# Kernel tuning notes

Measured on AMD Instinct MI355X. Metric: run time of the kernel, lower is better.

## Reference

```python
import jax, jax.numpy as jnp
import numpy as np

HIDDEN = 1024
NUM_HEADS = 16
HEAD_DIM = HIDDEN // NUM_HEADS
BATCH = 2
SEQ = 2048


def setup_inputs() -> dict:
    key = jax.random.key(0)
    k1, k2, k3 = jax.random.split(key, 3)
    hidden_states = jax.random.normal(k1, (BATCH, SEQ, HIDDEN), dtype=jnp.float32)
    attention_mask = jnp.zeros((BATCH, 1, SEQ, SEQ), dtype=jnp.float32)
    # nn.Linear weights: stored as [out_features, in_features]
    w_qkv = jax.random.normal(k2, (3 * HIDDEN, HIDDEN), dtype=jnp.float32) * (HIDDEN ** -0.5)
    w_o = jax.random.normal(k3, (HIDDEN, HIDDEN), dtype=jnp.float32) * (HIDDEN ** -0.5)
    return {"hidden_states": hidden_states, "attention_mask": attention_mask,
            "w_qkv": w_qkv, "w_o": w_o}


def reference(hidden_states, attention_mask, w_qkv, w_o):
    B, S, H = hidden_states.shape
    scale = HEAD_DIM ** -0.5
    qkv = jnp.einsum('bsh,oh->bso', hidden_states, w_qkv)  # [B,S,3H]
    qkv = qkv.reshape(B, S, 3, NUM_HEADS, HEAD_DIM)
    q = qkv[:, :, 0].transpose(0, 2, 1, 3)  # [B,nH,S,hd]
    k = qkv[:, :, 1].transpose(0, 2, 1, 3)
    v = qkv[:, :, 2].transpose(0, 2, 1, 3)
    attn = jnp.einsum('bhqd,bhkd->bhqk', q, k) * scale
    attn = attn + attention_mask
    attn = jax.nn.softmax(attn, axis=-1)
    out = jnp.einsum('bhqk,bhkd->bhqd', attn, v)
    out = out.transpose(0, 2, 1, 3).reshape(B, S, H)
    return jnp.einsum('bsh,oh->bso', out, w_o)
```

## Files before the change

kernel.cpp:

```cpp
#include <hip/hip_runtime.h>

typedef unsigned short u16;
using bf16x8 = __attribute__((ext_vector_type(8))) __bf16;
using f32x4  = __attribute__((ext_vector_type(4))) float;
using u16x8  = __attribute__((ext_vector_type(8))) unsigned short;
using u16x4  = __attribute__((ext_vector_type(4))) unsigned short;

#define SEQ   2048
#define HID   1024
#define NHEAD 16
#define HD    64
#define BATCH 2
#define NTOK  4096

__device__ __forceinline__ u16 f2bf(float f) {
  unsigned u = __builtin_bit_cast(unsigned, f);
  u += 0x7fffu + ((u >> 16) & 1u);
  return (u16)(u >> 16);
}

__device__ __forceinline__ void gld_lds16(const void* g, void* l) {
  __builtin_amdgcn_global_load_lds(
      (__attribute__((address_space(1))) void*)(__UINTPTR_TYPE__)g,
      (__attribute__((address_space(3))) void*)l, 16, 0, 0);
}

__global__ __launch_bounds__(256) void cvt_kernel(const float* __restrict__ in,
                                                  u16* __restrict__ out) {
  int i = (blockIdx.x * 256 + threadIdx.x) * 4;
  float4 v = *reinterpret_cast<const float4*>(in + i);
  u16x4 o = { f2bf(v.x), f2bf(v.y), f2bf(v.z), f2bf(v.w) };
  *reinterpret_cast<u16x4*>(out + i) = o;
}

template<bool BF16OUT>
__global__ __launch_bounds__(256) void gemm_bt(const u16* __restrict__ A,
                                               const u16* __restrict__ B,
                                               void* __restrict__ Cv,
                                               int M, int N, int K) {
  __shared__ u16 At[128 * 64];
  __shared__ u16 Bt[128 * 64];
  const int tid  = threadIdx.x;
  const int wave = tid >> 6;
  const int lane = tid & 63;
  const int g    = lane >> 4;
  const int r16  = lane & 15;
  const int wr   = wave >> 1;
  const int wc   = wave & 1;
  const int bm   = blockIdx.y;
  const int bn   = blockIdx.x;

  const u16* Ab = A + (size_t)bm * 128 * K;
  const u16* Bb = B + (size_t)bn * 128 * K;
  const int srow = lane >> 3;
  const int scol = (lane & 7) * 8;

  f32x4 acc[4][4] = {};

  for (int kt = 0; kt < K; kt += 64) {
#pragma unroll
    for (int c = 0; c < 4; ++c) {
      int seg = wave * 4 + c;
      gld_lds16(Ab + (size_t)(seg * 8 + srow) * K + kt + scol, &At[seg * 512]);
      gld_lds16(Bb + (size_t)(seg * 8 + srow) * K + kt + scol, &Bt[seg * 512]);
    }
    __syncthreads();
#pragma unroll
    for (int ko = 0; ko < 64; ko += 32) {
      bf16x8 af[4], bfr[4];
#pragma unroll
      for (int mi = 0; mi < 4; ++mi)
        af[mi] = *reinterpret_cast<const bf16x8*>(&At[(wr * 64 + mi * 16 + r16) * 64 + ko + g * 8]);
#pragma unroll
      for (int ni = 0; ni < 4; ++ni)
        bfr[ni] = *reinterpret_cast<const bf16x8*>(&Bt[(wc * 64 + ni * 16 + r16) * 64 + ko + g * 8]);
#pragma unroll
      for (int mi = 0; mi < 4; ++mi)
#pragma unroll
        for (int ni = 0; ni < 4; ++ni)
          acc[mi][ni] = __builtin_amdgcn_mfma_f32_16x16x32_bf16(af[mi], bfr[ni], acc[mi][ni], 0, 0, 0);
    }
    __syncthreads();
  }

#pragma unroll
  for (int mi = 0; mi < 4; ++mi)
#pragma unroll
    for (int ni = 0; ni < 4; ++ni) {
      int row0 = bm * 128 + wr * 64 + mi * 16 + g * 4;
      int col  = bn * 128 + wc * 64 + ni * 16 + r16;
#pragma unroll
      for (int r = 0; r < 4; ++r) {
        float v = acc[mi][ni][r];
        if (BF16OUT) ((u16*)Cv)[(size_t)(row0 + r) * N + col] = f2bf(v);
        else         ((float*)Cv)[(size_t)(row0 + r) * N + col] = v;
      }
    }
}

__global__ __launch_bounds__(256, 4) void attn_kernel(const u16* __restrict__ qkv,
                                                      const float* __restrict__ mask,
                                                      u16* __restrict__ AO) {
  __shared__ u16 Kt[2][64 * 64];
  __shared__ u16 Vt[64 * 64];
  __shared__ u16 Pl[4][16 * 64];

  const int tid  = threadIdx.x;
  const int w    = tid >> 6;
  const int lane = tid & 63;
  const int g    = lane >> 4;
  const int r16  = lane & 15;

  const int n  = blockIdx.x;
  const int x  = n & 7;
  const int s_ = n >> 3;
  const int h  = s_ & 15;
  const int t_ = ((s_ >> 4) << 3) + x;
  const int b  = t_ >> 5;
  const int qt = t_ & 31;

  const size_t tokbase = (size_t)b * SEQ;

  bf16x8 aq[2];
  {
    int qrow = qt * 64 + w * 16 + r16;
#pragma unroll
    for (int ko = 0; ko < 2; ++ko)
      aq[ko] = *reinterpret_cast<const bf16x8*>(
          qkv + ((tokbase + qrow) * 3 + 0) * HID + h * HD + ko * 32 + g * 8);
  }

  f32x4 o[4] = {};
  float mrow[4], lrow[4];
#pragma unroll
  for (int r = 0; r < 4; ++r) { mrow[r] = -3.0e38f; lrow[r] = 0.f; }

  const int srowK = lane >> 3;
  const int vkey  = tid >> 2;
  const int vd3   = tid & 3;

#define STAGE_K(buf, kb)                                                        \
  {                                                                             \
    _Pragma("unroll")                                                           \
    for (int c = 0; c < 2; ++c) {                                               \
      int seg = w * 2 + c;                                                      \
      int sK  = ((seg >> 1) + srowK) & 7;                                       \
      int srcc = (lane & 7) ^ sK;                                               \
      gld_lds16(qkv + ((tokbase + (kb) + seg * 8 + srowK) * 3 + 1) * HID +      \
                    h * HD + srcc * 8,                                          \
                &Kt[buf][seg * 512]);                                           \
    }                                                                           \
  }

  STAGE_K(0, 0);

#pragma unroll 1
  for (int kb = 0; kb < SEQ; kb += 64) {
    const int cur = (kb >> 6) & 1;
    const int nxt = cur ^ 1;
    const bool more = (kb + 64) < SEQ;

    float mpre[4][4];
#pragma unroll
    for (int r = 0; r < 4; ++r) {
      int q = qt * 64 + w * 16 + g * 4 + r;
      const float* mp = mask + ((size_t)b * SEQ + q) * SEQ + kb;
#pragma unroll
      for (int ni = 0; ni < 4; ++ni) mpre[r][ni] = mp[ni * 16 + r16];
    }
    const u16* vp = qkv + ((tokbase + kb + vkey) * 3 + 2) * HID + h * HD + vd3 * 16;
    u16x8 v0 = *reinterpret_cast<const u16x8*>(vp);
    u16x8 v1 = *reinterpret_cast<const u16x8*>(vp + 8);

    __syncthreads();

#pragma unroll
    for (int j = 0; j < 16; ++j) {
      u16 val = (j < 8) ? (u16)v0[j] : (u16)v1[j - 8];
      int row = vd3 * 16 + j;
      int sV  = (vd3 + (j & 7)) & 7;
      Vt[row * 64 + (((vkey >> 3) ^ sV) << 3) + (vkey & 7)] = val;
    }
    __syncthreads();

    f32x4 sf[4] = {};
#pragma unroll
    for (int ko = 0; ko < 2; ++ko) {
      bf16x8 bk[4];
#pragma unroll
      for (int ni = 0; ni < 4; ++ni) {
        int row = ni * 16 + r16;
        int sK  = (ni + (r16 & 7)) & 7;
        bk[ni] = *reinterpret_cast<const bf16x8*>(
            &Kt[cur][row * 64 + (((ko * 4 + g) ^ sK) << 3)]);
      }
#pragma unroll
      for (int ni = 0; ni < 4; ++ni)
        sf[ni] = __builtin_amdgcn_mfma_f32_16x16x32_bf16(aq[ko], bk[ni], sf[ni], 0, 0, 0);
    }

#pragma unroll
    for (int r = 0; r < 4; ++r) {
      float mx = -3.0e38f;
#pragma unroll
      for (int ni = 0; ni < 4; ++ni) {
        float sv = sf[ni][r] * 0.125f + mpre[r][ni];
        sf[ni][r] = sv;
        mx = fmaxf(mx, sv);
      }
      mx = fmaxf(mx, __shfl_xor(mx, 1));
      mx = fmaxf(mx, __shfl_xor(mx, 2));
      mx = fmaxf(mx, __shfl_xor(mx, 4));
      mx = fmaxf(mx, __shfl_xor(mx, 8));
      float mnew  = fmaxf(mrow[r], mx);
      float alpha = __expf(mrow[r] - mnew);
      mrow[r] = mnew;
      float s = 0.f;
#pragma unroll
      for (int ni = 0; ni < 4; ++ni) {
        float p = __expf(sf[ni][r] - mnew);
        sf[ni][r] = p;
        s += p;
      }
      s += __shfl_xor(s, 1); s += __shfl_xor(s, 2);
      s += __shfl_xor(s, 4); s += __shfl_xor(s, 8);
      lrow[r] = lrow[r] * alpha + s;
#pragma unroll
      for (int di = 0; di < 4; ++di) o[di][r] *= alpha;
      int prow = g * 4 + r;
      int sP   = prow & 7;
#pragma unroll
      for (int ni = 0; ni < 4; ++ni) {
        int chunk = ni * 2 + (r16 >> 3);
        Pl[w][prow * 64 + ((chunk ^ sP) << 3) + (r16 & 7)] = f2bf(sf[ni][r]);
      }
    }

    if (more) STAGE_K(nxt, kb + 64);

#pragma unroll
    for (int kk = 0; kk < 2; ++kk) {
      bf16x8 pa, bv[4];
      pa = *reinterpret_cast<const bf16x8*>(
          &Pl[w][r16 * 64 + (((kk * 4 + g) ^ (r16 & 7)) << 3)]);
#pragma unroll
      for (int di = 0; di < 4; ++di) {
        int row = di * 16 + r16;
        int sV  = (di + (r16 & 7)) & 7;
        bv[di] = *reinterpret_cast<const bf16x8*>(
            &Vt[row * 64 + (((kk * 4 + g) ^ sV) << 3)]);
      }
#pragma unroll
      for (int di = 0; di < 4; ++di)
        o[di] = __builtin_amdgcn_mfma_f32_16x16x32_bf16(pa, bv[di], o[di], 0, 0, 0);
    }
  }

#pragma unroll
  for (int di = 0; di < 4; ++di)
#pragma unroll
    for (int r = 0; r < 4; ++r) {
      int srow = qt * 64 + w * 16 + g * 4 + r;
      float val = o[di][r] / lrow[r];
      AO[(tokbase + srow) * HID + h * HD + di * 16 + r16] = f2bf(val);
    }
#undef STAGE_K
}

extern "C" void kernel_launch(void* const* d_in, const int* in_sizes, int n_in,
                              void* d_out, int out_size, void* d_ws, size_t ws_size,
                              hipStream_t stream) {
  (void)in_sizes; (void)n_in; (void)out_size; (void)ws_size;
  const float* hs   = (const float*)d_in[0];
  const float* mask = (const float*)d_in[1];
  const float* wqkv = (const float*)d_in[2];
  const float* wo   = (const float*)d_in[3];
  float* out = (float*)d_out;

  char* ws   = (char*)d_ws;
  u16* Xb    = (u16*)(ws);
  u16* Wqkvb = (u16*)(ws + 8u  * 1024 * 1024);
  u16* Wob   = (u16*)(ws + 14u * 1024 * 1024);
  u16* QKVb  = (u16*)(ws + 16u * 1024 * 1024);
  u16* AOb   = (u16*)(ws + 40u * 1024 * 1024);

  cvt_kernel<<<4096, 256, 0, stream>>>(hs,   Xb);
  cvt_kernel<<<3072, 256, 0, stream>>>(wqkv, Wqkvb);
  cvt_kernel<<<1024, 256, 0, stream>>>(wo,   Wob);

  gemm_bt<true ><<<dim3(3072 / 128, 4096 / 128), 256, 0, stream>>>(Xb,  Wqkvb, QKVb, NTOK, 3072, HID);
  attn_kernel   <<<1024, 256, 0, stream>>>(QKVb, mask, AOb);
  gemm_bt<false><<<dim3(1024 / 128, 4096 / 128), 256, 0, stream>>>(AOb, Wob,  out,  NTOK, 1024, HID);
}
```

Baseline: 208.5 us.

## Merge conversion launches, add 128x64 output GEMM, prioritize MFMA in attention

The three fp32-to-bf16 conversion launches become one kernel that picks its source by block index, removing two launch overheads. The output projection now uses a new 128x64-tile GEMM, which doubles the block count (512 instead of 256) so the 256 CUs are better filled. The attention kernel raises wave priority around its MFMA sections with s_setprio so that matrix work from different waves overlaps better. The new GEMM has no LDS swizzle, so it may suffer bank conflicts.

Result: faster. 198.3 us (-4.9%).

```diff
diff --git a/kernel.cpp b/kernel.cpp
--- a/kernel.cpp
+++ b/kernel.cpp
@@ -25,9 +25,15 @@
       (__attribute__((address_space(3))) void*)l, 16, 0, 0);
 }
 
-__global__ __launch_bounds__(256) void cvt_kernel(const float* __restrict__ in,
-                                                  u16* __restrict__ out) {
-  int i = (blockIdx.x * 256 + threadIdx.x) * 4;
+__global__ __launch_bounds__(256) void cvt3_kernel(const float* __restrict__ a, u16* __restrict__ oa,
+                                                   const float* __restrict__ b, u16* __restrict__ ob,
+                                                   const float* __restrict__ c, u16* __restrict__ oc) {
+  const float* in; u16* out; int off;
+  int bid = blockIdx.x;
+  if (bid < 4096)      { in = a; out = oa; off = bid; }
+  else if (bid < 7168) { in = b; out = ob; off = bid - 4096; }
+  else                 { in = c; out = oc; off = bid - 7168; }
+  int i = (off * 256 + threadIdx.x) * 4;
   float4 v = *reinterpret_cast<const float4*>(in + i);
   u16x4 o = { f2bf(v.x), f2bf(v.y), f2bf(v.z), f2bf(v.w) };
   *reinterpret_cast<u16x4*>(out + i) = o;
@@ -98,6 +104,69 @@
     }
 }
 
+__global__ __launch_bounds__(256) void gemm_bt64(const u16* __restrict__ A,
+                                                 const u16* __restrict__ B,
+                                                 float* __restrict__ C,
+                                                 int M, int N, int K) {
+  __shared__ u16 At[128 * 64];
+  __shared__ u16 Bt[64 * 64];
+  const int tid  = threadIdx.x;
+  const int wave = tid >> 6;
+  const int lane = tid & 63;
+  const int g    = lane >> 4;
+  const int r16  = lane & 15;
+  const int bm   = blockIdx.y;
+  const int bn   = blockIdx.x;
+
+  const u16* Ab = A + (size_t)bm * 128 * K;
+  const u16* Bb = B + (size_t)bn * 64 * K;
+  const int srow = lane >> 3;
+  const int scol = (lane & 7) * 8;
+
+  f32x4 acc[2][4] = {};
+
+  for (int kt = 0; kt < K; kt += 64) {
+#pragma unroll
+    for (int c = 0; c < 4; ++c) {
+      int seg = wave * 4 + c;
+      gld_lds16(Ab + (size_t)(seg * 8 + srow) * K + kt + scol, &At[seg * 512]);
+    }
+#pragma unroll
+    for (int c = 0; c < 2; ++c) {
+      int seg = wave * 2 + c;
+      gld_lds16(Bb + (size_t)(seg * 8 + srow) * K + kt + scol, &Bt[seg * 512]);
+    }
+    __syncthreads();
+#pragma unroll
+    for (int ko = 0; ko < 64; ko += 32) {
+      bf16x8 af[2], bfr[4];
+#pragma unroll
+      for (int mi = 0; mi < 2; ++mi)
+        af[mi] = *reinterpret_cast<const bf16x8*>(&At[(wave * 32 + mi * 16 + r16) * 64 + ko + g * 8]);
+#pragma unroll
+      for (int ni = 0; ni < 4; ++ni)
+        bfr[ni] = *reinterpret_cast<const bf16x8*>(&Bt[(ni * 16 + r16) * 64 + ko + g * 8]);
+#pragma unroll
+      for (int mi = 0; mi < 2; ++mi)
+#pragma unroll
+        for (int ni = 0; ni < 4; ++ni)
+          acc[mi][ni] = __builtin_amdgcn_mfma_f32_16x16x32_bf16(af[mi], bfr[ni], acc[mi][ni], 0, 0, 0);
+    }
+    __syncthreads();
+  }
+
+#pragma unroll
+  for (int mi = 0; mi < 2; ++mi)
+#pragma unroll
+    for (int ni = 0; ni < 4; ++ni) {
+      int row0 = bm * 128 + wave * 32 + mi * 16 + g * 4;
+      int col  = bn * 64 + ni * 16 + r16;
+#pragma unroll
+      for (int r = 0; r < 4; ++r)
+        C[(size_t)(row0 + r) * N + col] = acc[mi][ni][r];
+    }
+}
+
 __global__ __launch_bounds__(256, 4) void attn_kernel(const u16* __restrict__ qkv,
                                                       const float* __restrict__ mask,
                                                       u16* __restrict__ AO) {
@@ -184,6 +253,7 @@
     __syncthreads();
 
     f32x4 sf[4] = {};
+    __builtin_amdgcn_s_setprio(1);
 #pragma unroll
     for (int ko = 0; ko < 2; ++ko) {
       bf16x8 bk[4];
@@ -198,6 +268,7 @@
       for (int ni = 0; ni < 4; ++ni)
         sf[ni] = __builtin_amdgcn_mfma_f32_16x16x32_bf16(aq[ko], bk[ni], sf[ni], 0, 0, 0);
     }
+    __builtin_amdgcn_s_setprio(0);
 
 #pragma unroll
     for (int r = 0; r < 4; ++r) {
@@ -238,6 +309,7 @@
 
     if (more) STAGE_K(nxt, kb + 64);
 
+    __builtin_amdgcn_s_setprio(1);
 #pragma unroll
     for (int kk = 0; kk < 2; ++kk) {
       bf16x8 pa, bv[4];
@@ -254,6 +326,7 @@
       for (int di = 0; di < 4; ++di)
         o[di] = __builtin_amdgcn_mfma_f32_16x16x32_bf16(pa, bv[di], o[di], 0, 0, 0);
     }
+    __builtin_amdgcn_s_setprio(0);
   }
 
 #pragma unroll
@@ -284,11 +357,9 @@
   u16* QKVb  = (u16*)(ws + 16u * 1024 * 1024);
   u16* AOb   = (u16*)(ws + 40u * 1024 * 1024);
 
-  cvt_kernel<<<4096, 256, 0, stream>>>(hs,   Xb);
-  cvt_kernel<<<3072, 256, 0, stream>>>(wqkv, Wqkvb);
-  cvt_kernel<<<1024, 256, 0, stream>>>(wo,   Wob);
-
-  gemm_bt<true ><<<dim3(3072 / 128, 4096 / 128), 256, 0, stream>>>(Xb,  Wqkvb, QKVb, NTOK, 3072, HID);
-  attn_kernel   <<<1024, 256, 0, stream>>>(QKVb, mask, AOb);
-  gemm_bt<false><<<dim3(1024 / 128, 4096 / 128), 256, 0, stream>>>(AOb, Wob,  out,  NTOK, 1024, HID);
-}
+  cvt3_kernel<<<8192, 256, 0, stream>>>(hs, Xb, wqkv, Wqkvb, wo, Wob);
+
+  gemm_bt<true><<<dim3(3072 / 128, 4096 / 128), 256, 0, stream>>>(Xb, Wqkvb, QKVb, NTOK, 3072, HID);
+  attn_kernel  <<<1024, 256, 0, stream>>>(QKVb, mask, AOb);
+  gemm_bt64    <<<dim3(1024 / 64, 4096 / 128), 256, 0, stream>>>(AOb, Wob, out, NTOK, 1024, HID);
+}
```
